# Kernel optimization log

Measured on AMD Instinct MI355X. Metric: run time of the kernel, lower is better.

## Reference

```python
import jax, jax.numpy as jnp
import numpy as np

H = 768
IMG_DIM = 2048
B = 256
S = 512
EPS = 1e-5


def _ln(x, g, b):
    mu = jnp.mean(x, axis=-1, keepdims=True)
    var = jnp.var(x, axis=-1, keepdims=True)
    return (x - mu) * jax.lax.rsqrt(var + EPS) * g + b


def setup_inputs() -> dict:
    key = jax.random.key(0)
    ks = jax.random.split(key, 16)
    std = 0.02
    d = {
        "text_features": jax.random.normal(ks[0], (B, S, H), jnp.float32),
        "image_features": jax.random.normal(ks[1], (B, IMG_DIM), jnp.float32),
        # projections (stored as [in, out]); attention/proj weights init N(0, 0.02), zero bias
        "Wp": jax.random.normal(ks[2], (IMG_DIM, H), jnp.float32) * std,
        "bp": jnp.zeros((H,), jnp.float32),
        "Wtq": jax.random.normal(ks[3], (H, H), jnp.float32) * std,
        "btq": jnp.zeros((H,), jnp.float32),
        "Wik": jax.random.normal(ks[4], (H, H), jnp.float32) * std,
        "bik": jnp.zeros((H,), jnp.float32),
        "Wiv": jax.random.normal(ks[5], (H, H), jnp.float32) * std,
        "biv": jnp.zeros((H,), jnp.float32),
        "Wiq": jax.random.normal(ks[6], (H, H), jnp.float32) * std,
        "biq": jnp.zeros((H,), jnp.float32),
        "Wtk": jax.random.normal(ks[7], (H, H), jnp.float32) * std,
        "btk": jnp.zeros((H,), jnp.float32),
        "Wtv": jax.random.normal(ks[8], (H, H), jnp.float32) * std,
        "btv": jnp.zeros((H,), jnp.float32),
        # layernorms
        "tn_g": jnp.ones((H,), jnp.float32),
        "tn_b": jnp.zeros((H,), jnp.float32),
        "in_g": jnp.ones((H,), jnp.float32),
        "in_b": jnp.zeros((H,), jnp.float32),
        # fusion MLP: Linear(2H,H) + LN + GELU
        "Wf": jax.random.normal(ks[9], (2 * H, H), jnp.float32) * (1.0 / np.sqrt(2 * H)),
        "bf": jnp.zeros((H,), jnp.float32),
        "fn_g": jnp.ones((H,), jnp.float32),
        "fn_b": jnp.zeros((H,), jnp.float32),
        # gate: Linear(2H,2) + softmax
        "Wg": jax.random.normal(ks[10], (2 * H, 2), jnp.float32) * (1.0 / np.sqrt(2 * H)),
        "bg": jnp.zeros((2,), jnp.float32),
    }
    return d


def reference(text_features, image_features, Wp, bp, Wtq, btq, Wik, bik, Wiv, biv,
              Wiq, biq, Wtk, btk, Wtv, btv, tn_g, tn_b, in_g, in_b,
              Wf, bf, fn_g, fn_b, Wg, bg):
    scale = 1.0 / jnp.sqrt(jnp.float32(H))
    cls_token = text_features[:, 0]                       # [B, H]
    img_projected = image_features @ Wp + bp              # [B, H]

    # image query attends over text tokens
    img_q = img_projected @ Wiq + biq                     # [B, H]
    text_k = jnp.einsum('bsd,de->bse', text_features, Wtk) + btk  # [B, S, H]
    text_v = jnp.einsum('bsd,de->bse', text_features, Wtv) + btv  # [B, S, H]
    scores = jnp.einsum('bd,bsd->bs', img_q, text_k) * scale      # [B, S]
    attn = jax.nn.softmax(scores, axis=-1)
    img_context = jnp.einsum('bs,bsd->bd', attn, text_v)          # [B, H]
    img_context = _ln(img_context + img_projected, in_g, in_b)

    # text CLS query attends over the single image token (softmax over 1 -> weight 1)
    text_q = cls_token @ Wtq + btq                        # [B, H]
    img_k = img_projected @ Wik + bik                     # [B, H]
    img_v = img_projected @ Wiv + biv                     # [B, H]
    t_scores = jnp.sum(text_q * img_k, axis=-1, keepdims=True) * scale  # [B, 1]
    t_attn = jax.nn.softmax(t_scores, axis=-1)            # == 1
    text_context = t_attn * img_v                         # [B, H]
    text_context = _ln(text_context + cls_token, tn_g, tn_b)

    combined = jnp.concatenate([text_context, img_context], axis=1)  # [B, 2H]
    gate = jax.nn.softmax(combined @ Wg + bg, axis=-1)               # [B, 2]
    weighted = jnp.concatenate([text_context * gate[:, 0:1],
                                img_context * gate[:, 1:2]], axis=1)  # [B, 2H]
    out = jax.nn.gelu(_ln(weighted @ Wf + bf, fn_g, fn_b), approximate=False)
    return out
```

## Files before the change

kernel.cpp:

```cpp
#include <hip/hip_runtime.h>
#include <hip/hip_bf16.h>

#define BD   256
#define SD   512
#define HD   768
#define IMGD 2048
#define TWOH 1536
constexpr float EPSV  = 1e-5f;
constexpr float SCALE = 0.036084391824351615f;
constexpr int   SPLIT = 8;
constexpr int   SBLK  = SD / SPLIT;

typedef __attribute__((ext_vector_type(8))) short short8;
typedef __attribute__((ext_vector_type(4))) float f32x4;

__device__ __forceinline__ short f2bs(float x) {
    __hip_bfloat16 h = __float2bfloat16(x);
    return __builtin_bit_cast(short, h);
}
__device__ __forceinline__ float4 f4sum(float4 a, float4 b) {
    return make_float4(a.x + b.x, a.y + b.y, a.z + b.z, a.w + b.w);
}

struct GemmSmem {
    __hip_bfloat16 As[2][64][40];
    __hip_bfloat16 Bs[2][64][40];
};

template<bool TRANSB, class AF, class BF>
__device__ __forceinline__ void gemm_core(GemmSmem& smem, AF aload, BF bload,
        const float* __restrict__ bias, float* __restrict__ C,
        int N, int m0, int n0, int NT) {
    const int tid  = threadIdx.x;
    const int w    = tid >> 6, lane = tid & 63;
    const int wr   = w >> 1,  wc   = w & 1;
    const int rsel = lane & 15, ks = (lane >> 4) * 8;
    const int arow = tid >> 2, akc = (tid & 3) * 8;
    const int bkk  = tid >> 3, bnc = (tid & 7) * 8;

    float4 a0v[2], a1v[2], b0v[2], b1v[2];

    auto issue = [&](int slot, int t) {
        aload(t, a0v[slot], a1v[slot]);
        bload(t, b0v[slot], b1v[slot]);
    };
    auto commit = [&](int buf, int slot) {
        short8 pk;
        pk[0]=f2bs(a0v[slot].x); pk[1]=f2bs(a0v[slot].y);
        pk[2]=f2bs(a0v[slot].z); pk[3]=f2bs(a0v[slot].w);
        pk[4]=f2bs(a1v[slot].x); pk[5]=f2bs(a1v[slot].y);
        pk[6]=f2bs(a1v[slot].z); pk[7]=f2bs(a1v[slot].w);
        *(short8*)&smem.As[buf][arow][akc] = pk;
        if (TRANSB) {
            short8 qk;
            qk[0]=f2bs(b0v[slot].x); qk[1]=f2bs(b0v[slot].y);
            qk[2]=f2bs(b0v[slot].z); qk[3]=f2bs(b0v[slot].w);
            qk[4]=f2bs(b1v[slot].x); qk[5]=f2bs(b1v[slot].y);
            qk[6]=f2bs(b1v[slot].z); qk[7]=f2bs(b1v[slot].w);
            *(short8*)&smem.Bs[buf][arow][akc] = qk;
        } else {
            smem.Bs[buf][bnc + 0][bkk] = __float2bfloat16(b0v[slot].x);
            smem.Bs[buf][bnc + 1][bkk] = __float2bfloat16(b0v[slot].y);
            smem.Bs[buf][bnc + 2][bkk] = __float2bfloat16(b0v[slot].z);
            smem.Bs[buf][bnc + 3][bkk] = __float2bfloat16(b0v[slot].w);
            smem.Bs[buf][bnc + 4][bkk] = __float2bfloat16(b1v[slot].x);
            smem.Bs[buf][bnc + 5][bkk] = __float2bfloat16(b1v[slot].y);
            smem.Bs[buf][bnc + 6][bkk] = __float2bfloat16(b1v[slot].z);
            smem.Bs[buf][bnc + 7][bkk] = __float2bfloat16(b1v[slot].w);
        }
    };

    f32x4 zero = {0.f, 0.f, 0.f, 0.f};
    f32x4 acc[2][2] = {{zero, zero}, {zero, zero}};

    issue(0, 0);
    commit(0, 0);
    if (NT > 1) issue(1, 1);
    __syncthreads();

    for (int t = 0; t < NT; ++t) {
        const int cur = t & 1;
        short8 A0 = *(const short8*)&smem.As[cur][wr * 32 + rsel][ks];
        short8 A1 = *(const short8*)&smem.As[cur][wr * 32 + 16 + rsel][ks];
        short8 B0 = *(const short8*)&smem.Bs[cur][wc * 32 + rsel][ks];
        short8 B1 = *(const short8*)&smem.Bs[cur][wc * 32 + 16 + rsel][ks];
        if (t + 1 < NT) commit(cur ^ 1, (t + 1) & 1);
        if (t + 2 < NT) issue(cur, t + 2);
        acc[0][0] = __builtin_amdgcn_mfma_f32_16x16x32_bf16(A0, B0, acc[0][0], 0, 0, 0);
        acc[0][1] = __builtin_amdgcn_mfma_f32_16x16x32_bf16(A0, B1, acc[0][1], 0, 0, 0);
        acc[1][0] = __builtin_amdgcn_mfma_f32_16x16x32_bf16(A1, B0, acc[1][0], 0, 0, 0);
        acc[1][1] = __builtin_amdgcn_mfma_f32_16x16x32_bf16(A1, B1, acc[1][1], 0, 0, 0);
        __syncthreads();
    }

    const int colb = lane & 15, rowb = (lane >> 4) * 4;
    #pragma unroll
    for (int fm = 0; fm < 2; ++fm)
        #pragma unroll
        for (int fn = 0; fn < 2; ++fn)
            #pragma unroll
            for (int r = 0; r < 4; ++r) {
                int row = m0 + wr * 32 + fm * 16 + rowb + r;
                int col = n0 + wc * 32 + fn * 16 + colb;
                float v = acc[fm][fn][r];
                if (bias) v += bias[col];
                C[(size_t)row * N + col] = v;
            }
}

__global__ __launch_bounds__(256) void stage1(const float* __restrict__ imgf,
                                              const float* __restrict__ Wp,
                                              const float* __restrict__ bp,
                                              const float* __restrict__ Wiq,
                                              const float* __restrict__ Wtk,
                                              const float* __restrict__ biq,
                                              float* __restrict__ Pp,
                                              float* __restrict__ Wqkp,
                                              float* __restrict__ v1) {
    __shared__ GemmSmem smem;
    const int blk = blockIdx.x, tid = threadIdx.x;
    const int arow = tid >> 2, akc = (tid & 3) * 8;
    const int bkk  = tid >> 3, bnc = (tid & 7) * 8;
    if (blk < 192) {
        const int part = blk / 48, tile = blk % 48;
        const int m0 = (tile / 12) * 64, n0 = (tile % 12) * 64, kbeg = part * 512;
        const float* ap = &imgf[(size_t)(m0 + arow) * IMGD + kbeg + akc];
        const float* bq = &Wp[(size_t)(kbeg + bkk) * HD + n0 + bnc];
        auto al = [&](int t, float4& v0, float4& v1_) {
            const float* p = ap + t * 32;
            v0 = *(const float4*)p; v1_ = *(const float4*)(p + 4);
        };
        auto bl = [&](int t, float4& v0, float4& v1_) {
            const float* p = bq + (size_t)t * 32 * HD;
            v0 = *(const float4*)p; v1_ = *(const float4*)(p + 4);
        };
        gemm_core<false>(smem, al, bl, part == 0 ? bp : nullptr,
                         Pp + (size_t)part * BD * HD, HD, m0, n0, 16);
    } else if (blk < 480) {
        const int b2 = blk - 192, part = b2 / 144, tile = b2 % 144;
        const int m0 = (tile / 12) * 64, n0 = (tile % 12) * 64, kbeg = part * 384;
        const float* ap = &Wiq[(size_t)(m0 + arow) * HD + kbeg + akc];
        const float* bq = &Wtk[(size_t)(n0 + arow) * HD + kbeg + akc];
        auto al = [&](int t, float4& v0, float4& v1_) {
            const float* p = ap + t * 32;
            v0 = *(const float4*)p; v1_ = *(const float4*)(p + 4);
        };
        auto bl = [&](int t, float4& v0, float4& v1_) {
            const float* p = bq + t * 32;
            v0 = *(const float4*)p; v1_ = *(const float4*)(p + 4);
        };
        gemm_core<true>(smem, al, bl, nullptr,
                        Wqkp + (size_t)part * HD * HD, HD, m0, n0, 12);
    } else {
        const int b2 = blk - 480;
        const int w = tid >> 6, lane = tid & 63;
        float bq[12];
        #pragma unroll
        for (int c = 0; c < 12; ++c) bq[c] = biq[c * 64 + lane];
        const int d0 = b2 * 64 + w * 16;
        for (int i = 0; i < 16; ++i) {
            const float* row = &Wtk[(size_t)(d0 + i) * HD];
            float p = 0.f;
            #pragma unroll
            for (int c = 0; c < 12; ++c) p = fmaf(row[c * 64 + lane], bq[c], p);
            #pragma unroll
            for (int off = 32; off > 0; off >>= 1) p += __shfl_xor(p, off);
            if (lane == 0) v1[d0 + i] = p;
        }
    }
}

__global__ __launch_bounds__(256) void stage2(const float* __restrict__ Pp,
                                              const float* __restrict__ Wqkp,
                                              const float* __restrict__ v1,
                                              const float* __restrict__ Wiv,
                                              const float* __restrict__ biv,
                                              float* __restrict__ qtp,
                                              float* __restrict__ ivp) {
    __shared__ GemmSmem smem;
    const int blk = blockIdx.x, tid = threadIdx.x;
    const int arow = tid >> 2, akc = (tid & 3) * 8;
    const int bkk  = tid >> 3, bnc = (tid & 7) * 8;
    const bool isqt = blk < 96;
    const int b2 = isqt ? blk : blk - 96;
    const int part = b2 / 48, tile = b2 % 48;
    const int m0 = (tile / 12) * 64, n0 = (tile % 12) * 64, kbeg = part * 384;

    const float* ap = &Pp[(size_t)(m0 + arow) * HD + kbeg + akc];
    auto al = [&](int t, float4& v0, float4& v1_) {
        const float* p = ap + t * 32;
        float4 x0 = *(const float4*)p, x1 = *(const float4*)(p + 4);
        #pragma unroll
        for (int q = 1; q < 4; ++q) {
            const float* r = p + (size_t)q * BD * HD;
            x0 = f4sum(x0, *(const float4*)r);
            x1 = f4sum(x1, *(const float4*)(r + 4));
        }
        v0 = x0; v1_ = x1;
    };
    if (isqt) {
        const float* bq = &Wqkp[(size_t)(kbeg + bkk) * HD + n0 + bnc];
        auto bl = [&](int t, float4& v0, float4& v1_) {
            const float* p = bq + (size_t)t * 32 * HD;
            v0 = f4sum(*(const float4*)p, *(const float4*)(p + (size_t)HD * HD));
            v1_ = f4sum(*(const float4*)(p + 4), *(const float4*)(p + (size_t)HD * HD + 4));
        };
        gemm_core<false>(smem, al, bl, part == 0 ? v1 : nullptr,
                         qtp + (size_t)part * BD * HD, HD, m0, n0, 12);
    } else {
        const float* bq = &Wiv[(size_t)(kbeg + bkk) * HD + n0 + bnc];
        auto bl = [&](int t, float4& v0, float4& v1_) {
            const float* p = bq + (size_t)t * 32 * HD;
            v0 = *(const float4*)p; v1_ = *(const float4*)(p + 4);
        };
        gemm_core<false>(smem, al, bl, part == 0 ? biv : nullptr,
                         ivp + (size_t)part * BD * HD, HD, m0, n0, 12);
    }
}

__global__ __launch_bounds__(256) void gemm_ctxv(const float* __restrict__ ctx,
                                                 const float* __restrict__ Wtv,
                                                 const float* __restrict__ btv,
                                                 float* __restrict__ icpp) {
    __shared__ GemmSmem smem;
    const int tid = threadIdx.x;
    const int arow = tid >> 2, akc = (tid & 3) * 8;
    const int bkk  = tid >> 3, bnc = (tid & 7) * 8;
    const int part = blockIdx.x / 48, tile = blockIdx.x % 48;
    const int m0 = (tile / 12) * 64, n0 = (tile % 12) * 64, kbeg = part * 384;
    const float* ap = &ctx[(size_t)(m0 + arow) * HD + kbeg + akc];
    const float* bq = &Wtv[(size_t)(kbeg + bkk) * HD + n0 + bnc];
    auto al = [&](int t, float4& v0, float4& v1_) {
        const float* p = ap + t * 32;
        v0 = *(const float4*)p; v1_ = *(const float4*)(p + 4);
    };
    auto bl = [&](int t, float4& v0, float4& v1_) {
        const float* p = bq + (size_t)t * 32 * HD;
        v0 = *(const float4*)p; v1_ = *(const float4*)(p + 4);
    };
    gemm_core<false>(smem, al, bl, part == 0 ? btv : nullptr,
                     icpp + (size_t)part * BD * HD, HD, m0, n0, 12);
}

__global__ __launch_bounds__(256) void gemm_wf(const float* __restrict__ wtd,
                                               const float* __restrict__ Wf,
                                               const float* __restrict__ bf,
                                               float* __restrict__ ybp) {
    __shared__ GemmSmem smem;
    const int tid = threadIdx.x;
    const int arow = tid >> 2, akc = (tid & 3) * 8;
    const int bkk  = tid >> 3, bnc = (tid & 7) * 8;
    const int part = blockIdx.x / 48, tile = blockIdx.x % 48;
    const int m0 = (tile / 12) * 64, n0 = (tile % 12) * 64, kbeg = part * 384;
    const float* ap = &wtd[(size_t)(m0 + arow) * TWOH + kbeg + akc];
    const float* bq = &Wf[(size_t)(kbeg + bkk) * HD + n0 + bnc];
    auto al = [&](int t, float4& v0, float4& v1_) {
        const float* p = ap + t * 32;
        v0 = *(const float4*)p; v1_ = *(const float4*)(p + 4);
    };
    auto bl = [&](int t, float4& v0, float4& v1_) {
        const float* p = bq + (size_t)t * 32 * HD;
        v0 = *(const float4*)p; v1_ = *(const float4*)(p + 4);
    };
    gemm_core<false>(smem, al, bl, part == 0 ? bf : nullptr,
                     ybp + (size_t)part * BD * HD, HD, m0, n0, 12);
}

__global__ __launch_bounds__(256) void stream_attn(const float* __restrict__ tf,
                                                   const float* __restrict__ qtp,
                                                   float* __restrict__ pacc) {
    const int tid = threadIdx.x, w = tid >> 6, lane = tid & 63;
    __shared__ float sacc[4][HD];
    __shared__ float sm_[4], sl_[4];

    for (int item = blockIdx.x; item < BD * SPLIT; item += gridDim.x) {
        const int b = item / SPLIT, sl = item % SPLIT;

        float q[12];
        {
            const float* qp0 = &qtp[b * HD];
            const float* qp1 = qp0 + (size_t)BD * HD;
            #pragma unroll
            for (int c = 0; c < 3; ++c) {
                float4 v = f4sum(*(const float4*)&qp0[c * 256 + 4 * lane],
                                 *(const float4*)&qp1[c * 256 + 4 * lane]);
                q[c*4+0] = v.x; q[c*4+1] = v.y; q[c*4+2] = v.z; q[c*4+3] = v.w;
            }
        }
        float a[12];
        #pragma unroll
        for (int j = 0; j < 12; ++j) a[j] = 0.f;
        float m = -INFINITY, l = 0.f;

        const int r0 = sl * SBLK + w * (SBLK / 4);
        for (int i = 0; i < SBLK / 4; ++i) {
            const float* row = &tf[((size_t)b * SD + r0 + i) * HD];
            float t[12];
            #pragma unroll
            for (int c = 0; c < 3; ++c) {
                float4 v = *(const float4*)&row[c * 256 + 4 * lane];
                t[c*4+0] = v.x; t[c*4+1] = v.y; t[c*4+2] = v.z; t[c*4+3] = v.w;
            }
            float p = 0.f;
            #pragma unroll
            for (int j = 0; j < 12; ++j) p = fmaf(t[j], q[j], p);
            #pragma unroll
            for (int off = 32; off > 0; off >>= 1) p += __shfl_xor(p, off);
            float score = p * SCALE;
            if (score <= m) {
                float wt = expf(score - m);
                l += wt;
                #pragma unroll
                for (int j = 0; j < 12; ++j) a[j] = fmaf(wt, t[j], a[j]);
            } else {
                float f = expf(m - score);
                l = fmaf(l, f, 1.f);
                #pragma unroll
                for (int j = 0; j < 12; ++j) a[j] = fmaf(a[j], f, t[j]);
                m = score;
            }
        }
        #pragma unroll
        for (int c = 0; c < 3; ++c)
            #pragma unroll
            for (int j = 0; j < 4; ++j)
                sacc[w][c * 256 + 4 * lane + j] = a[c * 4 + j];
        if (lane == 0) { sm_[w] = m; sl_[w] = l; }
        __syncthreads();
        float gm = fmaxf(fmaxf(sm_[0], sm_[1]), fmaxf(sm_[2], sm_[3]));
        float f0 = expf(sm_[0] - gm), f1 = expf(sm_[1] - gm);
        float f2 = expf(sm_[2] - gm), f3 = expf(sm_[3] - gm);
        float gl = f0 * sl_[0] + f1 * sl_[1] + f2 * sl_[2] + f3 * sl_[3];
        float* outp = &pacc[(size_t)item * (HD + 2)];
        #pragma unroll
        for (int jj = 0; jj < 3; ++jj) {
            int c = jj * 256 + tid;
            outp[c] = f0 * sacc[0][c] + f1 * sacc[1][c] + f2 * sacc[2][c] + f3 * sacc[3][c];
        }
        if (tid == 0) { outp[HD] = gm; outp[HD + 1] = gl; }
        __syncthreads();
    }
}

__global__ __launch_bounds__(256) void merge_ctx(const float* __restrict__ pacc,
                                                 float* __restrict__ ctx) {
    const int b = blockIdx.x, tid = threadIdx.x;
    float gm = -INFINITY;
    #pragma unroll
    for (int s = 0; s < SPLIT; ++s)
        gm = fmaxf(gm, pacc[(size_t)(b * SPLIT + s) * (HD + 2) + HD]);
    float gl = 0.f, o0 = 0.f, o1 = 0.f, o2 = 0.f;
    #pragma unroll
    for (int s = 0; s < SPLIT; ++s) {
        const float* pp = &pacc[(size_t)(b * SPLIT + s) * (HD + 2)];
        float f = expf(pp[HD] - gm);
        gl += f * pp[HD + 1];
        o0 += f * pp[tid];
        o1 += f * pp[256 + tid];
        o2 += f * pp[512 + tid];
    }
    float inv = 1.f / gl;
    ctx[b * HD + tid]       = o0 * inv;
    ctx[b * HD + 256 + tid] = o1 * inv;
    ctx[b * HD + 512 + tid] = o2 * inv;
}

__device__ __forceinline__ float block_sum256(float v, float* red, int w, int lane) {
    #pragma unroll
    for (int off = 32; off > 0; off >>= 1) v += __shfl_xor(v, off);
    __syncthreads();
    if (lane == 0) red[w] = v;
    __syncthreads();
    return red[0] + red[1] + red[2] + red[3];
}

__global__ __launch_bounds__(256) void fuse_small(const float* __restrict__ icpp,
                                                  const float* __restrict__ Pp,
                                                  const float* __restrict__ ivp,
                                                  const float* __restrict__ tf,
                                                  const float* __restrict__ in_g,
                                                  const float* __restrict__ in_b,
                                                  const float* __restrict__ tn_g,
                                                  const float* __restrict__ tn_b,
                                                  const float* __restrict__ Wg,
                                                  const float* __restrict__ bg,
                                                  float* __restrict__ wtd) {
    const int b = blockIdx.x, tid = threadIdx.x;
    const int w = tid >> 6, lane = tid & 63;
    __shared__ float red[4];
    float icv[3], tcv[3];
    #pragma unroll
    for (int j = 0; j < 3; ++j) {
        int c = j * 256 + tid;
        float pv = 0.f;
        #pragma unroll
        for (int q = 0; q < 4; ++q) pv += Pp[(size_t)q * BD * HD + b * HD + c];
        float ic = icpp[b * HD + c] + icpp[(size_t)BD * HD + b * HD + c];
        icv[j] = ic + pv;
        float iv = ivp[b * HD + c] + ivp[(size_t)BD * HD + b * HD + c];
        tcv[j] = iv + tf[(size_t)b * SD * HD + c];
    }
    float s_i  = block_sum256(icv[0] + icv[1] + icv[2], red, w, lane);
    float ss_i = block_sum256(icv[0]*icv[0] + icv[1]*icv[1] + icv[2]*icv[2], red, w, lane);
    float s_t  = block_sum256(tcv[0] + tcv[1] + tcv[2], red, w, lane);
    float ss_t = block_sum256(tcv[0]*tcv[0] + tcv[1]*tcv[1] + tcv[2]*tcv[2], red, w, lane);
    const float invh = 1.f / HD;
    float mu_i = s_i * invh, var_i = ss_i * invh - mu_i * mu_i;
    float mu_t = s_t * invh, var_t = ss_t * invh - mu_t * mu_t;
    float rs_i = rsqrtf(var_i + EPSV), rs_t = rsqrtf(var_t + EPSV);
    float icn[3], tcn[3];
    #pragma unroll
    for (int j = 0; j < 3; ++j) {
        int c = j * 256 + tid;
        icn[j] = (icv[j] - mu_i) * rs_i * in_g[c] + in_b[c];
        tcn[j] = (tcv[j] - mu_t) * rs_t * tn_g[c] + tn_b[c];
    }
    float z0p = 0.f, z1p = 0.f;
    #pragma unroll
    for (int j = 0; j < 3; ++j) {
        int c = j * 256 + tid;
        z0p += tcn[j] * Wg[c * 2 + 0] + icn[j] * Wg[(HD + c) * 2 + 0];
        z1p += tcn[j] * Wg[c * 2 + 1] + icn[j] * Wg[(HD + c) * 2 + 1];
    }
    float z0 = block_sum256(z0p, red, w, lane) + bg[0];
    float z1 = block_sum256(z1p, red, w, lane) + bg[1];
    float mx = fmaxf(z0, z1);
    float e0 = expf(z0 - mx), e1 = expf(z1 - mx);
    float inv = 1.f / (e0 + e1);
    float g0 = e0 * inv, g1 = e1 * inv;
    #pragma unroll
    for (int j = 0; j < 3; ++j) {
        int c = j * 256 + tid;
        wtd[(size_t)b * TWOH + c]      = tcn[j] * g0;
        wtd[(size_t)b * TWOH + HD + c] = icn[j] * g1;
    }
}

__global__ __launch_bounds__(256) void final_ln_gelu(const float* __restrict__ ybp,
                                                     const float* __restrict__ fn_g,
                                                     const float* __restrict__ fn_b,
                                                     float* __restrict__ out) {
    const int b = blockIdx.x, tid = threadIdx.x;
    const int w = tid >> 6, lane = tid & 63;
    __shared__ float red[4];
    float v[3];
    #pragma unroll
    for (int j = 0; j < 3; ++j) {
        int c = j * 256 + tid;
        float x = 0.f;
        #pragma unroll
        for (int q = 0; q < 4; ++q) x += ybp[(size_t)q * BD * HD + b * HD + c];
        v[j] = x;
    }
    float s  = block_sum256(v[0] + v[1] + v[2], red, w, lane);
    float ss = block_sum256(v[0]*v[0] + v[1]*v[1] + v[2]*v[2], red, w, lane);
    const float invh = 1.f / HD;
    float mu = s * invh, var = ss * invh - mu * mu;
    float rs = rsqrtf(var + EPSV);
    #pragma unroll
    for (int j = 0; j < 3; ++j) {
        int c = j * 256 + tid;
        float x = (v[j] - mu) * rs * fn_g[c] + fn_b[c];
        float g = 0.5f * x * (1.f + erff(x * 0.7071067811865476f));
        out[b * HD + c] = g;
    }
}

extern "C" void kernel_launch(void* const* d_in, const int* in_sizes, int n_in,
                              void* d_out, int out_size, void* d_ws, size_t ws_size,
                              hipStream_t stream) {
    const float* tf   = (const float*)d_in[0];
    const float* imgf = (const float*)d_in[1];
    const float* Wp   = (const float*)d_in[2];
    const float* bp   = (const float*)d_in[3];
    const float* Wiv  = (const float*)d_in[8];
    const float* biv  = (const float*)d_in[9];
    const float* Wiq  = (const float*)d_in[10];
    const float* biq  = (const float*)d_in[11];
    const float* Wtk  = (const float*)d_in[12];
    const float* Wtv  = (const float*)d_in[14];
    const float* btv  = (const float*)d_in[15];
    const float* tn_g = (const float*)d_in[16];
    const float* tn_b = (const float*)d_in[17];
    const float* in_g = (const float*)d_in[18];
    const float* in_b = (const float*)d_in[19];
    const float* Wf   = (const float*)d_in[20];
    const float* bff  = (const float*)d_in[21];
    const float* fn_g = (const float*)d_in[22];
    const float* fn_b = (const float*)d_in[23];
    const float* Wg   = (const float*)d_in[24];
    const float* bg   = (const float*)d_in[25];

    float* ws    = (float*)d_ws;
    float* Pp    = ws;
    float* Wqkp  = Pp    + 4 * BD * HD;
    float* v1    = Wqkp  + 2 * HD * HD;
    float* qtp   = v1    + HD;
    float* ivp   = qtp   + 2 * BD * HD;
    float* ctx   = ivp   + 2 * BD * HD;
    float* icpp  = ctx   + BD * HD;
    float* ybp   = icpp  + 2 * BD * HD;
    float* wtd   = ybp   + 4 * BD * HD;
    float* pacc  = wtd   + BD * TWOH;

    stage1<<<492, 256, 0, stream>>>(imgf, Wp, bp, Wiq, Wtk, biq, Pp, Wqkp, v1);
    stage2<<<192, 256, 0, stream>>>(Pp, Wqkp, v1, Wiv, biv, qtp, ivp);
    stream_attn<<<1024, 256, 0, stream>>>(tf, qtp, pacc);
    merge_ctx<<<BD, 256, 0, stream>>>(pacc, ctx);
    gemm_ctxv<<<96, 256, 0, stream>>>(ctx, Wtv, btv, icpp);
    fuse_small<<<BD, 256, 0, stream>>>(icpp, Pp, ivp, tf, in_g, in_b, tn_g, tn_b,
                                       Wg, bg, wtd);
    gemm_wf<<<192, 256, 0, stream>>>(wtd, Wf, bff, ybp);
    final_ln_gelu<<<BD, 256, 0, stream>>>(ybp, fn_g, fn_b, (float*)d_out);
}
```

Baseline: 145.3 us.

## Fuse split-softmax merge into ctx GEMM A-load and halve attention split count

Removes the merge_ctx kernel by having gemm_ctxv compute per-row split weights from stored (max, sum) pairs and combine the partial accumulators while loading its A tile. The attention split drops from 8 to 4 and the grid-stride loop is replaced with one item per block. The inner loop gains two-row register prefetch and a branchless online-softmax update using __expf. This saves a launch and the ctx round trip to memory. In exchange there are fewer attention blocks, so occupancy is lower, and the GEMM A-load repeats the weighted combine in every N tile.

```diff
diff --git a/kernel.cpp b/kernel.cpp
--- a/kernel.cpp
+++ b/kernel.cpp
@@ -8,7 +8,7 @@
 #define TWOH 1536
 constexpr float EPSV  = 1e-5f;
 constexpr float SCALE = 0.036084391824351615f;
-constexpr int   SPLIT = 8;
+constexpr int   SPLIT = 4;
 constexpr int   SBLK  = SD / SPLIT;
 
 typedef __attribute__((ext_vector_type(8))) short short8;
@@ -20,6 +20,10 @@
 }
 __device__ __forceinline__ float4 f4sum(float4 a, float4 b) {
     return make_float4(a.x + b.x, a.y + b.y, a.z + b.z, a.w + b.w);
+}
+__device__ __forceinline__ float4 f4fma(float s, float4 v, float4 acc) {
+    return make_float4(fmaf(s, v.x, acc.x), fmaf(s, v.y, acc.y),
+                       fmaf(s, v.z, acc.z), fmaf(s, v.w, acc.w));
 }
 
 struct GemmSmem {
@@ -218,22 +222,133 @@
     }
 }
 
-__global__ __launch_bounds__(256) void gemm_ctxv(const float* __restrict__ ctx,
+__global__ __launch_bounds__(256) void stream_attn(const float* __restrict__ tf,
+                                                   const float* __restrict__ qtp,
+                                                   float* __restrict__ pacc,
+                                                   float* __restrict__ ml) {
+    const int tid = threadIdx.x, w = tid >> 6, lane = tid & 63;
+    const int item = blockIdx.x;
+    const int b = item >> 2, sl = item & 3;
+    __shared__ float sacc[4][HD];
+    __shared__ float sm_[4], sl_[4];
+
+    float q[12];
+    {
+        const float* qp0 = &qtp[b * HD];
+        const float* qp1 = qp0 + (size_t)BD * HD;
+        #pragma unroll
+        for (int c = 0; c < 3; ++c) {
+            float4 v = f4sum(*(const float4*)&qp0[c * 256 + 4 * lane],
+                             *(const float4*)&qp1[c * 256 + 4 * lane]);
+            q[c*4+0] = v.x; q[c*4+1] = v.y; q[c*4+2] = v.z; q[c*4+3] = v.w;
+        }
+    }
+    float a[12];
+    #pragma unroll
+    for (int j = 0; j < 12; ++j) a[j] = 0.f;
+    float m = -INFINITY, l = 0.f;
+
+    const int r0 = sl * SBLK + w * (SBLK / 4);
+    const float* base = &tf[((size_t)b * SD + r0) * HD];
+
+    float tA[12], tB[12];
+    auto loadrow = [&](int i, float* t) {
+        const float* row = base + (size_t)i * HD;
+        #pragma unroll
+        for (int c = 0; c < 3; ++c) {
+            float4 v = *(const float4*)&row[c * 256 + 4 * lane];
+            t[c*4+0] = v.x; t[c*4+1] = v.y; t[c*4+2] = v.z; t[c*4+3] = v.w;
+        }
+    };
+    auto process = [&](const float* t) {
+        float p = 0.f;
+        #pragma unroll
+        for (int j = 0; j < 12; ++j) p = fmaf(t[j], q[j], p);
+        #pragma unroll
+        for (int off = 32; off > 0; off >>= 1) p += __shfl_xor(p, off);
+        float score = p * SCALE;
+        float mn = fmaxf(m, score);
+        float eo = __expf(m - mn);
+        float en = __expf(score - mn);
+        l = fmaf(l, eo, en);
+        #pragma unroll
+        for (int j = 0; j < 12; ++j) a[j] = fmaf(a[j], eo, en * t[j]);
+        m = mn;
+    };
+
+    loadrow(0, tA);
+    for (int i = 0; i < 32; i += 2) {
+        loadrow(i + 1, tB);
+        process(tA);
+        if (i + 2 < 32) loadrow(i + 2, tA);
+        process(tB);
+    }
+
+    #pragma unroll
+    for (int c = 0; c < 3; ++c)
+        #pragma unroll
+        for (int j = 0; j < 4; ++j)
+            sacc[w][c * 256 + 4 * lane + j] = a[c * 4 + j];
+    if (lane == 0) { sm_[w] = m; sl_[w] = l; }
+    __syncthreads();
+    float gm = fmaxf(fmaxf(sm_[0], sm_[1]), fmaxf(sm_[2], sm_[3]));
+    float f0 = __expf(sm_[0] - gm), f1 = __expf(sm_[1] - gm);
+    float f2 = __expf(sm_[2] - gm), f3 = __expf(sm_[3] - gm);
+    float gl = f0 * sl_[0] + f1 * sl_[1] + f2 * sl_[2] + f3 * sl_[3];
+    float* outp = &pacc[(size_t)item * HD];
+    #pragma unroll
+    for (int jj = 0; jj < 3; ++jj) {
+        int c = jj * 256 + tid;
+        outp[c] = f0 * sacc[0][c] + f1 * sacc[1][c] + f2 * sacc[2][c] + f3 * sacc[3][c];
+    }
+    if (tid == 0) { ml[item * 2] = gm; ml[item * 2 + 1] = gl; }
+}
+
+__global__ __launch_bounds__(256) void gemm_ctxv(const float* __restrict__ pacc,
+                                                 const float* __restrict__ ml,
                                                  const float* __restrict__ Wtv,
                                                  const float* __restrict__ btv,
                                                  float* __restrict__ icpp) {
     __shared__ GemmSmem smem;
+    __shared__ float wgt[64][SPLIT];
     const int tid = threadIdx.x;
     const int arow = tid >> 2, akc = (tid & 3) * 8;
     const int bkk  = tid >> 3, bnc = (tid & 7) * 8;
     const int part = blockIdx.x / 48, tile = blockIdx.x % 48;
     const int m0 = (tile / 12) * 64, n0 = (tile % 12) * 64, kbeg = part * 384;
-    const float* ap = &ctx[(size_t)(m0 + arow) * HD + kbeg + akc];
-    const float* bq = &Wtv[(size_t)(kbeg + bkk) * HD + n0 + bnc];
+
+    if (tid < 64) {
+        const int gr = m0 + tid;
+        float mv[SPLIT], lv[SPLIT];
+        #pragma unroll
+        for (int s = 0; s < SPLIT; ++s) {
+            mv[s] = ml[(gr * SPLIT + s) * 2];
+            lv[s] = ml[(gr * SPLIT + s) * 2 + 1];
+        }
+        float mx = fmaxf(fmaxf(mv[0], mv[1]), fmaxf(mv[2], mv[3]));
+        float f[SPLIT], gl = 0.f;
+        #pragma unroll
+        for (int s = 0; s < SPLIT; ++s) { f[s] = __expf(mv[s] - mx); gl += f[s] * lv[s]; }
+        float inv = 1.f / gl;
+        #pragma unroll
+        for (int s = 0; s < SPLIT; ++s) wgt[tid][s] = f[s] * inv;
+    }
+    __syncthreads();
+
+    const float* ap = &pacc[(size_t)(m0 + arow) * SPLIT * HD + kbeg + akc];
     auto al = [&](int t, float4& v0, float4& v1_) {
         const float* p = ap + t * 32;
-        v0 = *(const float4*)p; v1_ = *(const float4*)(p + 4);
-    };
+        float4 x0 = {0.f, 0.f, 0.f, 0.f}, x1 = {0.f, 0.f, 0.f, 0.f};
+        #pragma unroll
+        for (int s = 0; s < SPLIT; ++s) {
+            float wv = wgt[arow][s];
+            const float* r = p + (size_t)s * HD;
+            x0 = f4fma(wv, *(const float4*)r, x0);
+            x1 = f4fma(wv, *(const float4*)(r + 4), x1);
+        }
+        v0 = x0; v1_ = x1;
+    };
+    const float* bq = &Wtv[(size_t)(kbeg + bkk) * HD + n0 + bnc];
     auto bl = [&](int t, float4& v0, float4& v1_) {
         const float* p = bq + (size_t)t * 32 * HD;
         v0 = *(const float4*)p; v1_ = *(const float4*)(p + 4);
@@ -266,105 +381,6 @@
                      ybp + (size_t)part * BD * HD, HD, m0, n0, 12);
 }
 
-__global__ __launch_bounds__(256) void stream_attn(const float* __restrict__ tf,
-                                                   const float* __restrict__ qtp,
-                                                   float* __restrict__ pacc) {
-    const int tid = threadIdx.x, w = tid >> 6, lane = tid & 63;
-    __shared__ float sacc[4][HD];
-    __shared__ float sm_[4], sl_[4];
-
-    for (int item = blockIdx.x; item < BD * SPLIT; item += gridDim.x) {
-        const int b = item / SPLIT, sl = item % SPLIT;
-
-        float q[12];
-        {
-            const float* qp0 = &qtp[b * HD];
-            const float* qp1 = qp0 + (size_t)BD * HD;
-            #pragma unroll
-            for (int c = 0; c < 3; ++c) {
-                float4 v = f4sum(*(const float4*)&qp0[c * 256 + 4 * lane],
-                                 *(const float4*)&qp1[c * 256 + 4 * lane]);
-                q[c*4+0] = v.x; q[c*4+1] = v.y; q[c*4+2] = v.z; q[c*4+3] = v.w;
-            }
-        }
-        float a[12];
-        #pragma unroll
-        for (int j = 0; j < 12; ++j) a[j] = 0.f;
-        float m = -INFINITY, l = 0.f;
-
-        const int r0 = sl * SBLK + w * (SBLK / 4);
-        for (int i = 0; i < SBLK / 4; ++i) {
-            const float* row = &tf[((size_t)b * SD + r0 + i) * HD];
-            float t[12];
-            #pragma unroll
-            for (int c = 0; c < 3; ++c) {
-                float4 v = *(const float4*)&row[c * 256 + 4 * lane];
-                t[c*4+0] = v.x; t[c*4+1] = v.y; t[c*4+2] = v.z; t[c*4+3] = v.w;
-            }
-            float p = 0.f;
-            #pragma unroll
-            for (int j = 0; j < 12; ++j) p = fmaf(t[j], q[j], p);
-            #pragma unroll
-            for (int off = 32; off > 0; off >>= 1) p += __shfl_xor(p, off);
-            float score = p * SCALE;
-            if (score <= m) {
-                float wt = expf(score - m);
-                l += wt;
-                #pragma unroll
-                for (int j = 0; j < 12; ++j) a[j] = fmaf(wt, t[j], a[j]);
-            } else {
-                float f = expf(m - score);
-                l = fmaf(l, f, 1.f);
-                #pragma unroll
-                for (int j = 0; j < 12; ++j) a[j] = fmaf(a[j], f, t[j]);
-                m = score;
-            }
-        }
-        #pragma unroll
-        for (int c = 0; c < 3; ++c)
-            #pragma unroll
-            for (int j = 0; j < 4; ++j)
-                sacc[w][c * 256 + 4 * lane + j] = a[c * 4 + j];
-        if (lane == 0) { sm_[w] = m; sl_[w] = l; }
-        __syncthreads();
-        float gm = fmaxf(fmaxf(sm_[0], sm_[1]), fmaxf(sm_[2], sm_[3]));
-        float f0 = expf(sm_[0] - gm), f1 = expf(sm_[1] - gm);
-        float f2 = expf(sm_[2] - gm), f3 = expf(sm_[3] - gm);
-        float gl = f0 * sl_[0] + f1 * sl_[1] + f2 * sl_[2] + f3 * sl_[3];
-        float* outp = &pacc[(size_t)item * (HD + 2)];
-        #pragma unroll
-        for (int jj = 0; jj < 3; ++jj) {
-            int c = jj * 256 + tid;
-            outp[c] = f0 * sacc[0][c] + f1 * sacc[1][c] + f2 * sacc[2][c] + f3 * sacc[3][c];
-        }
-        if (tid == 0) { outp[HD] = gm; outp[HD + 1] = gl; }
-        __syncthreads();
-    }
-}
-
-__global__ __launch_bounds__(256) void merge_ctx(const float* __restrict__ pacc,
-                                                 float* __restrict__ ctx) {
-    const int b = blockIdx.x, tid = threadIdx.x;
-    float gm = -INFINITY;
-    #pragma unroll
-    for (int s = 0; s < SPLIT; ++s)
-        gm = fmaxf(gm, pacc[(size_t)(b * SPLIT + s) * (HD + 2) + HD]);
-    float gl = 0.f, o0 = 0.f, o1 = 0.f, o2 = 0.f;
-    #pragma unroll
-    for (int s = 0; s < SPLIT; ++s) {
-        const float* pp = &pacc[(size_t)(b * SPLIT + s) * (HD + 2)];
-        float f = expf(pp[HD] - gm);
-        gl += f * pp[HD + 1];
-        o0 += f * pp[tid];
-        o1 += f * pp[256 + tid];
-        o2 += f * pp[512 + tid];
-    }
-    float inv = 1.f / gl;
-    ctx[b * HD + tid]       = o0 * inv;
-    ctx[b * HD + 256 + tid] = o1 * inv;
-    ctx[b * HD + 512 + tid] = o2 * inv;
-}
-
 __device__ __forceinline__ float block_sum256(float v, float* red, int w, int lane) {
     #pragma unroll
     for (int off = 32; off > 0; off >>= 1) v += __shfl_xor(v, off);
@@ -425,7 +441,7 @@
     float z0 = block_sum256(z0p, red, w, lane) + bg[0];
     float z1 = block_sum256(z1p, red, w, lane) + bg[1];
     float mx = fmaxf(z0, z1);
-    float e0 = expf(z0 - mx), e1 = expf(z1 - mx);
+    float e0 = __expf(z0 - mx), e1 = __expf(z1 - mx);
     float inv = 1.f / (e0 + e1);
     float g0 = e0 * inv, g1 = e1 * inv;
     #pragma unroll
@@ -497,17 +513,16 @@
     float* v1    = Wqkp  + 2 * HD * HD;
     float* qtp   = v1    + HD;
     float* ivp   = qtp   + 2 * BD * HD;
-    float* ctx   = ivp   + 2 * BD * HD;
-    float* icpp  = ctx   + BD * HD;
+    float* icpp  = ivp   + 2 * BD * HD;
     float* ybp   = icpp  + 2 * BD * HD;
     float* wtd   = ybp   + 4 * BD * HD;
     float* pacc  = wtd   + BD * TWOH;
+    float* ml    = pacc  + (size_t)BD * SPLIT * HD;
 
     stage1<<<492, 256, 0, stream>>>(imgf, Wp, bp, Wiq, Wtk, biq, Pp, Wqkp, v1);
     stage2<<<192, 256, 0, stream>>>(Pp, Wqkp, v1, Wiv, biv, qtp, ivp);
-    stream_attn<<<1024, 256, 0, stream>>>(tf, qtp, pacc);
-    merge_ctx<<<BD, 256, 0, stream>>>(pacc, ctx);
-    gemm_ctxv<<<96, 256, 0, stream>>>(ctx, Wtv, btv, icpp);
+    stream_attn<<<BD * SPLIT, 256, 0, stream>>>(tf, qtp, pacc, ml);
+    gemm_ctxv<<<96, 256, 0, stream>>>(pacc, ml, Wtv, btv, icpp);
     fuse_small<<<BD, 256, 0, stream>>>(icpp, Pp, ivp, tf, in_g, in_b, tn_g, tn_b,
                                        Wg, bg, wtd);
     gemm_wf<<<192, 256, 0, stream>>>(wtd, Wf, bff, ybp);
```

Result: no change. 145.7 us, median of 2 (+0.3%).
